# Kernel optimization log

Measured on AMD Instinct MI355X. Metric: run time of the kernel, lower is better.

Reference implementation:

```python
import jax, jax.numpy as jnp
import numpy as np

K = 3            # kernel size (odd)
CO, CI = 16, 16  # out/in channels

def setup_inputs() -> dict:
    key = jax.random.key(0)
    k1, k2, k3, k4 = jax.random.split(key, 4)
    B, C, H, W = 4, CI, 128, 128
    input_data = jax.random.normal(k1, (B, C, H, W), dtype=jnp.float32)
    # fixation coordinates in pixel units
    foa_xy = jax.random.uniform(k2, (B, 2), dtype=jnp.float32) * jnp.array([W, H], jnp.float32)
    hidden = 256
    W1 = jax.random.normal(k3, (2, hidden), dtype=jnp.float32) * (1.0 / jnp.sqrt(2.0))
    b1 = jnp.zeros((hidden,), jnp.float32)
    W2 = jax.random.normal(k4, (hidden, CO * CI * K * K), dtype=jnp.float32) * (1.0 / jnp.sqrt(hidden))
    b2 = jnp.zeros((CO * CI * K * K,), jnp.float32)
    return {"input_data": input_data, "foa_xy": foa_xy, "W1": W1, "b1": b1, "W2": W2, "b2": b2}

def _unfold_reflect(x, k):
    # x: [B, C, H, W] -> patches [B, C, k*k, H*W], reflect padding, stride 1, dilation 1
    B, C, H, W = x.shape
    pad = (k - 1) // 2
    xp = jnp.pad(x, ((0, 0), (0, 0), (pad, pad), (pad, pad)), mode="reflect")
    rows = [xp[:, :, i:i + H, j:j + W] for i in range(k) for j in range(k)]
    return jnp.stack(rows, axis=2).reshape(B, C, k * k, H * W)

def reference(input_data, foa_xy, W1, b1, W2, b2):
    B, C, H, W = input_data.shape
    # coordinate grid [H*W, 2] as (x, y), matching torch meshgrid(ij) + stack(xx, yy)
    ys = jnp.arange(H, dtype=jnp.float32)
    xs = jnp.arange(W, dtype=jnp.float32)
    yy, xx = jnp.meshgrid(ys, xs, indexing="ij")
    coords = jnp.stack([xx.ravel(), yy.ravel()], axis=1)         # [HW, 2]
    net_in = (coords[None, :, :] - foa_xy[:, None, :]).reshape(B * H * W, 2)
    # kernel-generating MLP
    h = jax.nn.relu(net_in @ W1 + b1)
    net_out = h @ W2 + b2                                        # [B*HW, CO*CI*K*K]
    kernel = net_out.reshape(B, H * W, CO, CI, K * K)            # [B, P, o, i, q]
    patches = _unfold_reflect(input_data, K)                     # [B, CI, K*K, HW]
    # per-pixel conv: sum over in-channels and kernel taps
    out = jnp.einsum("biqp,bpoiq->bop", patches, kernel)         # [B, CO, HW]
    return out.reshape(B, CO, H, W)
```

## Files before the change

kernel.cpp:

```cpp
#include <hip/hip_runtime.h>

#define CI    16
#define CO    16
#define HID   256
#define KPAD  288
#define NKK   9
#define NKH   8
#define NCH   144
#define IMGH  128
#define IMGW  128
#define NMS   8
#define RSTR  132
#define RLEN  130
#define KKSTR (NCH * 32)
#define OSTRS (NKK * NCH * 32)

typedef float f32x4  __attribute__((ext_vector_type(4)));
typedef float f32x2  __attribute__((ext_vector_type(2)));
typedef short bf16x8 __attribute__((ext_vector_type(8)));

__device__ __host__ __forceinline__ short f2bf(float f) {
  union { float f; unsigned u; } c; c.f = f;
  unsigned b = c.u + 0x7FFFu + ((c.u >> 16) & 1u);
  return (short)(b >> 16);
}

__global__ void prep_w2(const float* __restrict__ W2, const float* __restrict__ b2,
                        short* __restrict__ W2b) {
  __shared__ float tile[32][65];
  const int kk = blockIdx.x % NKK;
  const int colbase = (blockIdx.x / NKK) * 64;
  const int tid = threadIdx.x;

  for (int e = tid; e < 2048; e += 256) {
    int klr = e >> 6;
    int cc  = e & 63;
    int col = colbase + cc;
    float v;
    if (kk < 8) v = W2[(kk * 32 + klr) * (CO * NCH) + col];
    else        v = (klr == 0) ? b2[col] : 0.f;
    tile[klr][cc] = v;
  }
  __syncthreads();
  for (int e = tid; e < 2048; e += 256) {
    int cc = e >> 5;
    int kl = e & 31;
    int col = colbase + cc;
    int o = col / NCH;
    int n = col - o * NCH;
    int i = n / 9, q = n - i * 9;
    int dyr = q / 3, dx = q - dyr * 3;
    int np = dx * 48 + i * 3 + dyr;
    W2b[(((o * NKK + kk) * NCH + np) << 5) + kl] = f2bf(tile[kl][cc]);
  }
}

__global__ __launch_bounds__(256, 2)
void ngconv_main(const float* __restrict__ in, const float* __restrict__ foa,
                 const float* __restrict__ W1, const float* __restrict__ b1,
                 const short* __restrict__ W2b, float* __restrict__ out) {
  __shared__ short shHf[64 * 512];
  __shared__ short shPatch[48 * RSTR];

  const int tid  = threadIdx.x;
  const int lane = tid & 63;
  const int wv   = tid >> 6;
  const int c15  = lane & 15;
  const int quad = lane >> 4;

  const int blk = blockIdx.x;
  const int b   = blk >> 7;
  const int y   = blk & 127;

  const float fx  = foa[b * 2 + 0];
  const float fy  = foa[b * 2 + 1];
  const float dyv = (float)y - fy;

  const int ry0 = (y == 0) ? 1 : (y - 1);
  const int ry2 = (y == IMGH - 1) ? (IMGH - 2) : (y + 1);

  for (int e = tid; e < 48 * RLEN; e += 256) {
    int r  = e / RLEN;
    int xx = e - r * RLEN;
    int i = r / 3, dyr = r - i * 3;
    int ryr = (dyr == 0) ? ry0 : ((dyr == 1) ? y : ry2);
    int x = xx - 1;
    x = (x < 0) ? 1 : ((x > IMGW - 1) ? (IMGW - 2) : x);
    shPatch[r * RSTR + xx] = f2bf(in[((b * CI + i) * IMGH + ryr) * IMGW + x]);
  }

  for (int g = tid; g < 128 * 32; g += 256) {
    int px = g & 127;
    int ks = g >> 7;
    int k0 = ks << 3;
    float dxv = (float)px - fx;
    short hv[8];
    #pragma unroll
    for (int j = 0; j < 8; ++j) {
      int k = k0 + j;
      float h = fmaxf(fmaf(dxv, W1[k], fmaf(dyv, W1[HID + k], b1[k])), 0.f);
      hv[j] = f2bf(h);
    }
    int ms = px >> 4;
    int kk = k0 >> 5;
    int lslot = ((k0 & 31) >> 3) * 16 + (px & 15);
    *(bf16x8*)&shHf[((ms * NKH + kk) << 9) + (lslot << 3)] = *(bf16x8*)hv;
  }

  bf16x8 af8 = (bf16x8){0, 0, 0, 0, 0, 0, 0, 0};
  if (quad == 0) af8[0] = (short)0x3F80;

  __syncthreads();

  #pragma unroll 1
  for (int oj = 0; oj < 4; ++oj) {
    const int o = wv + oj * 4;
    const short* Bo = W2b + o * OSTRS + (c15 << 5) + (quad << 3);

    f32x2 P2[16];
    #pragma unroll
    for (int t = 0; t < 16; ++t) P2[t] = (f32x2){0.f, 0.f};

    #pragma unroll 1
    for (int pass = 0; pass < 3; ++pass) {
      const short* Bp = Bo + (pass * 3) * 512;
      f32x4 acc[NMS][3];
      #pragma unroll
      for (int ms = 0; ms < NMS; ++ms)
        #pragma unroll
        for (int j = 0; j < 3; ++j)
          acc[ms][j] = (f32x4){0.f, 0.f, 0.f, 0.f};

      bf16x8 bE[3], bO[3];
      #pragma unroll
      for (int j = 0; j < 3; ++j) bE[j] = *(const bf16x8*)&Bp[j << 9];

      #pragma unroll 1
      for (int t = 0; t < 4; ++t) {
        const int kkE = 2 * t;
        #pragma unroll
        for (int j = 0; j < 3; ++j)
          bO[j] = *(const bf16x8*)&Bp[(kkE + 1) * KKSTR + (j << 9)];
        {
          const short* hp = shHf + (kkE << 9) + (lane << 3);
          #pragma unroll
          for (int ms = 0; ms < NMS; ++ms) {
            bf16x8 af = *(const bf16x8*)&hp[ms * (NKH << 9)];
            #pragma unroll
            for (int j = 0; j < 3; ++j)
              acc[ms][j] = __builtin_amdgcn_mfma_f32_16x16x32_bf16(
                  af, bE[j], acc[ms][j], 0, 0, 0);
          }
        }
        #pragma unroll
        for (int j = 0; j < 3; ++j)
          bE[j] = *(const bf16x8*)&Bp[(kkE + 2) * KKSTR + (j << 9)];
        {
          const short* hp = shHf + ((kkE + 1) << 9) + (lane << 3);
          #pragma unroll
          for (int ms = 0; ms < NMS; ++ms) {
            bf16x8 af = *(const bf16x8*)&hp[ms * (NKH << 9)];
            #pragma unroll
            for (int j = 0; j < 3; ++j)
              acc[ms][j] = __builtin_amdgcn_mfma_f32_16x16x32_bf16(
                  af, bO[j], acc[ms][j], 0, 0, 0);
          }
        }
      }
      {
        #pragma unroll
        for (int ms = 0; ms < NMS; ++ms)
          #pragma unroll
          for (int j = 0; j < 3; ++j)
            acc[ms][j] = __builtin_amdgcn_mfma_f32_16x16x32_bf16(
                af8, bE[j], acc[ms][j], 0, 0, 0);
      }

      const int sh = pass << 4;
      #pragma unroll
      for (int j = 0; j < 3; ++j) {
        const short* prow = &shPatch[((j << 4) + c15) * RSTR + (quad << 2)];
        #pragma unroll
        for (int ms = 0; ms < NMS; ++ms) {
          uint2 u0 = *(const uint2*)&prow[ms * 16];
          unsigned u1 = *(const unsigned*)&prow[ms * 16 + 4];
          unsigned long long a0 =
              (unsigned long long)u0.x | ((unsigned long long)u0.y << 32);
          unsigned long long a1 =
              (unsigned long long)u0.y | ((unsigned long long)u1 << 32);
          unsigned d0 = (unsigned)(a0 >> sh);
          unsigned d1 = (unsigned)(a1 >> sh);
          float p0 = __uint_as_float(d0 << 16);
          float p1 = __uint_as_float(d0 & 0xFFFF0000u);
          float p2 = __uint_as_float(d1 << 16);
          float p3 = __uint_as_float(d1 & 0xFFFF0000u);
          f32x2 a01 = {acc[ms][j][0], acc[ms][j][1]};
          f32x2 a23 = {acc[ms][j][2], acc[ms][j][3]};
          P2[ms * 2 + 0] += a01 * (f32x2){p0, p1};
          P2[ms * 2 + 1] += a23 * (f32x2){p2, p3};
        }
      }
    }

    #pragma unroll
    for (int half = 0; half < 2; ++half) {
      float P[16];
      #pragma unroll
      for (int t = 0; t < 16; ++t) P[t] = P2[half * 8 + (t >> 1)][t & 1];
      #pragma unroll
      for (int m = 8; m >= 1; m >>= 1) {
        const bool hi = (c15 & m) != 0;
        #pragma unroll
        for (int j = 0; j < m; ++j) {
          float keep = hi ? P[j + m] : P[j];
          float send = hi ? P[j] : P[j + m];
          float recv = __shfl_xor(send, m, 64);
          P[j] = keep + recv;
        }
      }
      const int x = half * 64 + (c15 >> 2) * 16 + quad * 4 + (c15 & 3);
      out[((b * CO + o) * IMGH + y) * IMGW + x] = P[0];
    }
  }
}

extern "C" void kernel_launch(void* const* d_in, const int* in_sizes, int n_in,
                              void* d_out, int out_size, void* d_ws, size_t ws_size,
                              hipStream_t stream) {
  const float* in  = (const float*)d_in[0];
  const float* foa = (const float*)d_in[1];
  const float* W1  = (const float*)d_in[2];
  const float* b1  = (const float*)d_in[3];
  const float* W2  = (const float*)d_in[4];
  const float* b2  = (const float*)d_in[5];
  float* out = (float*)d_out;
  short* W2b = (short*)d_ws;

  prep_w2<<<324, 256, 0, stream>>>(W2, b2, W2b);
  ngconv_main<<<512, 256, 0, stream>>>(in, foa, W1, b1, W2b, out);
}
```

Baseline: 155.8 us.

## Split pixel row across two wave groups with 512-thread blocks

Doubles the block to 8 waves and splits the 128-pixel row into two 64-pixel halves, one per wave group. Each wave now keeps 4 M-subtiles of accumulators instead of 8, which cuts register pressure and allows higher launch bounds occupancy. The cost is that each wave group streams the same W2 B-fragments from global memory, so B-load traffic per pixel doubles. LDS use per block is unchanged.

Measured after the change: 188.1 us. 20.8% more time.

```diff
diff --git a/kernel.cpp b/kernel.cpp
--- a/kernel.cpp
+++ b/kernel.cpp
@@ -14,6 +14,7 @@
 #define RLEN  130
 #define KKSTR (NCH * 32)
 #define OSTRS (NKK * NCH * 32)
+#define MGOFF (4 * NKH * 512)
 
 typedef float f32x4  __attribute__((ext_vector_type(4)));
 typedef float f32x2  __attribute__((ext_vector_type(2)));
@@ -55,7 +56,7 @@
   }
 }
 
-__global__ __launch_bounds__(256, 2)
+__global__ __launch_bounds__(512, 4)
 void ngconv_main(const float* __restrict__ in, const float* __restrict__ foa,
                  const float* __restrict__ W1, const float* __restrict__ b1,
                  const short* __restrict__ W2b, float* __restrict__ out) {
@@ -64,7 +65,9 @@
 
   const int tid  = threadIdx.x;
   const int lane = tid & 63;
-  const int wv   = tid >> 6;
+  const int wv8  = tid >> 6;
+  const int mg   = wv8 >> 2;
+  const int wo   = wv8 & 3;
   const int c15  = lane & 15;
   const int quad = lane >> 4;
 
@@ -79,7 +82,7 @@
   const int ry0 = (y == 0) ? 1 : (y - 1);
   const int ry2 = (y == IMGH - 1) ? (IMGH - 2) : (y + 1);
 
-  for (int e = tid; e < 48 * RLEN; e += 256) {
+  for (int e = tid; e < 48 * RLEN; e += 512) {
     int r  = e / RLEN;
     int xx = e - r * RLEN;
     int i = r / 3, dyr = r - i * 3;
@@ -89,7 +92,7 @@
     shPatch[r * RSTR + xx] = f2bf(in[((b * CI + i) * IMGH + ryr) * IMGW + x]);
   }
 
-  for (int g = tid; g < 128 * 32; g += 256) {
+  for (int g = tid; g < 128 * 32; g += 512) {
     int px = g & 127;
     int ks = g >> 7;
     int k0 = ks << 3;
@@ -112,21 +115,23 @@
 
   __syncthreads();
 
+  const short* shHg = shHf + mg * MGOFF;
+
   #pragma unroll 1
   for (int oj = 0; oj < 4; ++oj) {
-    const int o = wv + oj * 4;
+    const int o = wo + oj * 4;
     const short* Bo = W2b + o * OSTRS + (c15 << 5) + (quad << 3);
 
-    f32x2 P2[16];
-    #pragma unroll
-    for (int t = 0; t < 16; ++t) P2[t] = (f32x2){0.f, 0.f};
+    f32x2 P2[8];
+    #pragma unroll
+    for (int t = 0; t < 8; ++t) P2[t] = (f32x2){0.f, 0.f};
 
     #pragma unroll 1
     for (int pass = 0; pass < 3; ++pass) {
       const short* Bp = Bo + (pass * 3) * 512;
-      f32x4 acc[NMS][3];
-      #pragma unroll
-      for (int ms = 0; ms < NMS; ++ms)
+      f32x4 acc[4][3];
+      #pragma unroll
+      for (int ms = 0; ms < 4; ++ms)
         #pragma unroll
         for (int j = 0; j < 3; ++j)
           acc[ms][j] = (f32x4){0.f, 0.f, 0.f, 0.f};
@@ -142,9 +147,9 @@
         for (int j = 0; j < 3; ++j)
           bO[j] = *(const bf16x8*)&Bp[(kkE + 1) * KKSTR + (j << 9)];
         {
-          const short* hp = shHf + (kkE << 9) + (lane << 3);
+          const short* hp = shHg + (kkE << 9) + (lane << 3);
           #pragma unroll
-          for (int ms = 0; ms < NMS; ++ms) {
+          for (int ms = 0; ms < 4; ++ms) {
             bf16x8 af = *(const bf16x8*)&hp[ms * (NKH << 9)];
             #pragma unroll
             for (int j = 0; j < 3; ++j)
@@ -156,9 +161,9 @@
         for (int j = 0; j < 3; ++j)
           bE[j] = *(const bf16x8*)&Bp[(kkE + 2) * KKSTR + (j << 9)];
         {
-          const short* hp = shHf + ((kkE + 1) << 9) + (lane << 3);
+          const short* hp = shHg + ((kkE + 1) << 9) + (lane << 3);
           #pragma unroll
-          for (int ms = 0; ms < NMS; ++ms) {
+          for (int ms = 0; ms < 4; ++ms) {
             bf16x8 af = *(const bf16x8*)&hp[ms * (NKH << 9)];
             #pragma unroll
             for (int j = 0; j < 3; ++j)
@@ -169,7 +174,7 @@
       }
       {
         #pragma unroll
-        for (int ms = 0; ms < NMS; ++ms)
+        for (int ms = 0; ms < 4; ++ms)
           #pragma unroll
           for (int j = 0; j < 3; ++j)
             acc[ms][j] = __builtin_amdgcn_mfma_f32_16x16x32_bf16(
@@ -179,9 +184,9 @@
       const int sh = pass << 4;
       #pragma unroll
       for (int j = 0; j < 3; ++j) {
-        const short* prow = &shPatch[((j << 4) + c15) * RSTR + (quad << 2)];
-        #pragma unroll
-        for (int ms = 0; ms < NMS; ++ms) {
+        const short* prow = &shPatch[((j << 4) + c15) * RSTR + (mg << 6) + (quad << 2)];
+        #pragma unroll
+        for (int ms = 0; ms < 4; ++ms) {
           uint2 u0 = *(const uint2*)&prow[ms * 16];
           unsigned u1 = *(const unsigned*)&prow[ms * 16 + 4];
           unsigned long long a0 =
@@ -202,25 +207,23 @@
       }
     }
 
-    #pragma unroll
-    for (int half = 0; half < 2; ++half) {
-      float P[16];
-      #pragma unroll
-      for (int t = 0; t < 16; ++t) P[t] = P2[half * 8 + (t >> 1)][t & 1];
-      #pragma unroll
-      for (int m = 8; m >= 1; m >>= 1) {
-        const bool hi = (c15 & m) != 0;
-        #pragma unroll
-        for (int j = 0; j < m; ++j) {
-          float keep = hi ? P[j + m] : P[j];
-          float send = hi ? P[j] : P[j + m];
-          float recv = __shfl_xor(send, m, 64);
-          P[j] = keep + recv;
-        }
-      }
-      const int x = half * 64 + (c15 >> 2) * 16 + quad * 4 + (c15 & 3);
-      out[((b * CO + o) * IMGH + y) * IMGW + x] = P[0];
+    float P[16];
+    #pragma unroll
+    for (int t = 0; t < 16; ++t) P[t] = P2[t >> 1][t & 1];
+    #pragma unroll
+    for (int m = 8; m >= 1; m >>= 1) {
+      const bool hi = (c15 & m) != 0;
+      #pragma unroll
+      for (int j = 0; j < m; ++j) {
+        float keep = hi ? P[j + m] : P[j];
+        float send = hi ? P[j] : P[j + m];
+        float recv = __shfl_xor(send, m, 64);
+        P[j] = keep + recv;
+      }
     }
+
+    const int x = (mg << 6) + (c15 >> 2) * 16 + quad * 4 + (c15 & 3);
+    out[((b * CO + o) * IMGH + y) * IMGW + x] = P[0];
   }
 }
 
@@ -237,5 +240,5 @@
   short* W2b = (short*)d_ws;
 
   prep_w2<<<324, 256, 0, stream>>>(W2, b2, W2b);
-  ngconv_main<<<512, 256, 0, stream>>>(in, foa, W1, b1, W2b, out);
-}
+  ngconv_main<<<512, 512, 0, stream>>>(in, foa, W1, b1, W2b, out);
+}
```
